# Optimization experiments

Hardware: AMD Instinct MI355X
Metric: run time of the kernel (lower is better)

The kernel has to match this reference:

```python
import jax, jax.numpy as jnp
import numpy as np

B, S, D, H, DH, DM = 2, 2048, 1024, 16, 64, 4096
EPS = 1e-5
IGNORE = -100000.0
INIT_RANGE = 0.02


def setup_inputs() -> dict:
    key = jax.random.key(0)
    ks = jax.random.split(key, 8)
    inp = {
        "resid_pre": jax.random.normal(ks[0], (B, S, D), jnp.float32),
        "ln1_w": jnp.ones((D,), jnp.float32),
        "ln1_b": jnp.zeros((D,), jnp.float32),
        "W_Q": jax.random.normal(ks[1], (H, D, DH), jnp.float32) * 0.05,
        "b_Q": jnp.zeros((H, DH), jnp.float32),
        "W_K": jax.random.normal(ks[2], (H, D, DH), jnp.float32) * 0.05,
        "b_K": jnp.zeros((H, DH), jnp.float32),
        "W_V": jax.random.normal(ks[3], (H, D, DH), jnp.float32) * 0.05,
        "b_V": jnp.zeros((H, DH), jnp.float32),
        "W_O": jax.random.normal(ks[4], (H, DH, D), jnp.float32) * 0.05,
        "b_O": jnp.zeros((D,), jnp.float32),
        "ln2_w": jnp.ones((D,), jnp.float32),
        "ln2_b": jnp.zeros((D,), jnp.float32),
        "W_in": jax.random.normal(ks[5], (D, DM), jnp.float32) * INIT_RANGE,
        "b_in": jnp.zeros((DM,), jnp.float32),
        "W_out": jax.random.normal(ks[6], (DM, D), jnp.float32) * INIT_RANGE,
        "b_out": jnp.zeros((D,), jnp.float32),
    }
    return inp


def _layernorm(x, w, b):
    mean = jnp.mean(x, axis=-1, keepdims=True)
    xc = x - mean
    var = jnp.mean(jnp.square(xc), axis=-1, keepdims=True)
    return xc / jnp.sqrt(var + EPS) * w + b


def _attention(x, W_Q, b_Q, W_K, b_K, W_V, b_V, W_O, b_O):
    q = jnp.einsum('bqd,hdm->bqhm', x, W_Q) + b_Q
    k = jnp.einsum('bkd,hdm->bkhm', x, W_K) + b_K
    scores = jnp.einsum('bqhd,bkhd->bhqk', q, k) / jnp.sqrt(jnp.float32(DH))
    s = x.shape[1]
    causal = jnp.tril(jnp.ones((s, s), bool))  # True = keep
    scores = jnp.where(causal, scores, IGNORE)
    pattern = jax.nn.softmax(scores, axis=-1)
    v = jnp.einsum('bkd,hdm->bkhm', x, W_V) + b_V
    z = jnp.einsum('bhqk,bkhd->bqhd', pattern, v)
    return jnp.einsum('bqhd,hdm->bqm', z, W_O) + b_O


def reference(resid_pre, ln1_w, ln1_b, W_Q, b_Q, W_K, b_K, W_V, b_V, W_O, b_O,
              ln2_w, ln2_b, W_in, b_in, W_out, b_out):
    # Pre-LN attention + residual (dropout disabled: inference mode)
    attn_out = _attention(_layernorm(resid_pre, ln1_w, ln1_b),
                          W_Q, b_Q, W_K, b_K, W_V, b_V, W_O, b_O)
    resid_mid = resid_pre + attn_out
    # Pre-LN MLP + residual; keras gelu default is exact (erf-based)
    h = _layernorm(resid_mid, ln2_w, ln2_b)
    pre = jnp.einsum('bpd,dm->bpm', h, W_in) + b_in
    post = jax.nn.gelu(pre, approximate=False)
    mlp_out = jnp.einsum('bpm,md->bpd', post, W_out) + b_out
    return resid_mid + mlp_out
```

## Files before the change

### kernel.cpp

```cpp
#include <hip/hip_runtime.h>
#include <math.h>

#define S_LEN   2048
#define D_MODEL 1024
#define N_HEADS 16
#define D_HEAD  64
#define D_MLP   4096
#define T_TOKENS 4096
#define QSCALE_F 0.18033688011112042f

typedef __attribute__((ext_vector_type(8))) short short8;
typedef __attribute__((ext_vector_type(4))) float f32x4;
typedef unsigned short ushort_t;
typedef unsigned long long u64;

__device__ __forceinline__ ushort_t f2bf(float x) {
    unsigned int u = __float_as_uint(x);
    return (ushort_t)((u + 0x7FFFu + ((u >> 16) & 1u)) >> 16);
}

__device__ __forceinline__ float gelu_exact(float x) {
    return 0.5f * x * (1.0f + erff(x * 0.7071067811865476f));
}

__device__ __forceinline__ void gld_lds16(const void* g, void* l) {
    __builtin_amdgcn_global_load_lds(
        (const __attribute__((address_space(1))) unsigned int*)g,
        (__attribute__((address_space(3))) unsigned int*)l, 16, 0, 0);
}

__device__ __forceinline__ void swizzle_mn(int& m0, int& n0) {
    int gx = gridDim.x;
    int b = blockIdx.y * gx + blockIdx.x;
    int band = b & 7, t = b >> 3;
    n0 = (t % gx) * 128;
    m0 = (band * 4 + t / gx) * 128;
}


__global__ __launch_bounds__(256) void ln_kernel(const float* __restrict__ x,
                                                 const float* __restrict__ w,
                                                 const float* __restrict__ b,
                                                 ushort_t* __restrict__ out) {
    int t = blockIdx.x;
    int tid = threadIdx.x;
    const float* xp = x + (size_t)t * D_MODEL;
    float4 v = *(const float4*)(xp + tid * 4);
    float s  = v.x + v.y + v.z + v.w;
    float sq = v.x*v.x + v.y*v.y + v.z*v.z + v.w*v.w;
    for (int o = 32; o; o >>= 1) {
        s  += __shfl_down(s, o, 64);
        sq += __shfl_down(sq, o, 64);
    }
    __shared__ float ss[4], ssq[4];
    if ((tid & 63) == 0) { ss[tid >> 6] = s; ssq[tid >> 6] = sq; }
    __syncthreads();
    float S  = ss[0] + ss[1] + ss[2] + ss[3];
    float SQ = ssq[0] + ssq[1] + ssq[2] + ssq[3];
    float mean = S * (1.0f / D_MODEL);
    float var  = SQ * (1.0f / D_MODEL) - mean * mean;
    float rstd = rsqrtf(var + 1e-5f);
    float4 wv = *(const float4*)(w + tid * 4);
    float4 bv = *(const float4*)(b + tid * 4);
    float ox = (v.x - mean) * rstd * wv.x + bv.x;
    float oy = (v.y - mean) * rstd * wv.y + bv.y;
    float oz = (v.z - mean) * rstd * wv.z + bv.z;
    float ow = (v.w - mean) * rstd * wv.w + bv.w;
    u64 pack = (u64)f2bf(ox) | ((u64)f2bf(oy) << 16) | ((u64)f2bf(oz) << 32) | ((u64)f2bf(ow) << 48);
    *(u64*)(out + (size_t)t * D_MODEL + tid * 4) = pack;
}

__global__ __launch_bounds__(256) void transpose_f2b(const float* __restrict__ in,
                                                     long long inStride, int ldin,
                                                     ushort_t* __restrict__ out,
                                                     long long outStride, int ldout) {
    in  += (size_t)blockIdx.z * inStride;
    out += (size_t)blockIdx.z * outStride;
    __shared__ float t[32][33];
    int c0 = blockIdx.x * 32, r0 = blockIdx.y * 32;
    int tx = threadIdx.x, ty = threadIdx.y;
    #pragma unroll
    for (int i = 0; i < 32; i += 8)
        t[ty + i][tx] = in[(size_t)(r0 + ty + i) * ldin + c0 + tx];
    __syncthreads();
    #pragma unroll
    for (int i = 0; i < 32; i += 8)
        out[(size_t)(c0 + ty + i) * ldout + r0 + tx] = f2bf(t[tx][ty + i]);
}

__global__ __launch_bounds__(256) void tpose_b2b(const ushort_t* __restrict__ in,
                                                 ushort_t* __restrict__ out) {
    int pair = blockIdx.z;
    in  += (size_t)pair * (S_LEN * 64);
    out += (size_t)pair * (S_LEN * 64);
    __shared__ ushort_t t[32][33];
    int s0 = blockIdx.x * 32, d0 = blockIdx.y * 32;
    int tx = threadIdx.x, ty = threadIdx.y;
    #pragma unroll
    for (int i = 0; i < 32; i += 8)
        t[ty + i][tx] = in[(size_t)(s0 + ty + i) * 64 + d0 + tx];
    __syncthreads();
    #pragma unroll
    for (int i = 0; i < 32; i += 8)
        out[(size_t)(d0 + ty + i) * S_LEN + s0 + tx] = t[tx][ty + i];
}

__global__ __launch_bounds__(256) void qkv_bias_cat(const float* __restrict__ bq,
                                                    const float* __restrict__ bk,
                                                    const float* __restrict__ bv,
                                                    float* __restrict__ out) {
    int i = blockIdx.x * 256 + threadIdx.x;
    float v = (i < 1024) ? bq[i] : (i < 2048 ? bk[i - 1024] : bv[i - 2048]);
    out[i] = v;
}

template<int OUT_MODE, bool DO_GELU, bool HAS_RES>
__global__ __launch_bounds__(256, 4) void mfma_gemm(
    const ushort_t* __restrict__ A, int lda,
    const ushort_t* __restrict__ Bt, int ldb,
    void* __restrict__ Cv, int ldc, int K,
    const float* __restrict__ bias,
    const float* __restrict__ res, int ldres) {

    __shared__ ushort_t As[2][128 * 32];
    __shared__ ushort_t Bs[2][128 * 32];

    int tid  = threadIdx.x;
    int lane = tid & 63;
    int m0, n0;
    swizzle_mn(m0, n0);
    int wave = tid >> 6;
    int wm = (wave & 1) * 64, wn = (wave >> 1) * 64;
    int quad = lane >> 4, l15 = lane & 15;

    int srow = tid >> 2;
    int skc  = (((tid & 3) ^ ((tid >> 3) & 3))) * 8;
    const ushort_t* Ap  = A  + (size_t)(m0 + srow)      * lda + skc;
    const ushort_t* Ap2 = A  + (size_t)(m0 + srow + 64) * lda + skc;
    const ushort_t* Bp  = Bt + (size_t)(n0 + srow)      * ldb + skc;
    const ushort_t* Bp2 = Bt + (size_t)(n0 + srow + 64) * ldb + skc;

    int fsw = (l15 >> 1) & 3;

    f32x4 acc[4][4];
    #pragma unroll
    for (int i = 0; i < 4; ++i)
        #pragma unroll
        for (int j = 0; j < 4; ++j)
            acc[i][j] = (f32x4){0.f, 0.f, 0.f, 0.f};

    gld_lds16(Ap,  &As[0][tid * 8]);
    gld_lds16(Ap2, &As[0][(tid + 256) * 8]);
    gld_lds16(Bp,  &Bs[0][tid * 8]);
    gld_lds16(Bp2, &Bs[0][(tid + 256) * 8]);

    int niter = K >> 5;
    for (int j = 0; j < niter; ++j) {
        __syncthreads();
        int p = j & 1;
        if (j + 1 < niter) {
            int k1 = (j + 1) << 5;
            gld_lds16(Ap  + k1, &As[p ^ 1][tid * 8]);
            gld_lds16(Ap2 + k1, &As[p ^ 1][(tid + 256) * 8]);
            gld_lds16(Bp  + k1, &Bs[p ^ 1][tid * 8]);
            gld_lds16(Bp2 + k1, &Bs[p ^ 1][(tid + 256) * 8]);
        }
        short8 a[4], b[4];
        #pragma unroll
        for (int i = 0; i < 4; ++i) {
            a[i] = *(const short8*)&As[p][(wm + i * 16 + l15) * 32 + (quad ^ fsw) * 8];
            b[i] = *(const short8*)&Bs[p][(wn + i * 16 + l15) * 32 + (quad ^ fsw) * 8];
        }
        #pragma unroll
        for (int i = 0; i < 4; ++i)
            #pragma unroll
            for (int jj = 0; jj < 4; ++jj)
                acc[i][jj] = __builtin_amdgcn_mfma_f32_16x16x32_bf16(a[i], b[jj], acc[i][jj], 0, 0, 0);
    }

    #pragma unroll
    for (int i = 0; i < 4; ++i) {
        int rBase = m0 + wm + i * 16 + quad * 4;
        #pragma unroll
        for (int j = 0; j < 4; ++j) {
            int col = n0 + wn + j * 16 + l15;
            float bv = bias ? bias[col] : 0.f;
            #pragma unroll
            for (int r = 0; r < 4; ++r) {
                int rowg = rBase + r;
                float v = acc[i][j][r] + bv;
                if (DO_GELU) v = gelu_exact(v);
                if (HAS_RES) v += res[(size_t)rowg * ldres + col];
                if (OUT_MODE == 0)
                    ((float*)Cv)[(size_t)rowg * ldc + col] = v;
                else
                    ((ushort_t*)Cv)[(size_t)rowg * ldc + col] = f2bf(v);
            }
        }
    }
}

template<int OUT_MODE, bool DO_GELU, bool HAS_RES>
__global__ __launch_bounds__(512, 2) void mfma_gemm_sk(
    const ushort_t* __restrict__ A, int lda,
    const ushort_t* __restrict__ Bt, int ldb,
    void* __restrict__ Cv, int ldc, int K,
    const float* __restrict__ bias,
    const float* __restrict__ res, int ldres) {

    __shared__ ushort_t Smem[32768];
    #define SA_(g, p) (Smem + ((g) * 2 + (p)) * 4096)
    #define SB_(g, p) (Smem + 16384 + ((g) * 2 + (p)) * 4096)

    int tid  = threadIdx.x;
    int lane = tid & 63;
    int wave = tid >> 6;
    int g = wave >> 2, w = wave & 3;
    int m0, n0;
    swizzle_mn(m0, n0);
    int wm = (w & 1) * 64, wn = (w >> 1) * 64;
    int quad = lane >> 4, l15 = lane & 15;

    int lt = tid & 255;
    int srow = lt >> 2;
    int skc  = (((lt & 3) ^ ((lt >> 3) & 3))) * 8;
    int kbase = g * (K >> 1);
    const ushort_t* Ap  = A  + (size_t)(m0 + srow)      * lda + kbase + skc;
    const ushort_t* Ap2 = A  + (size_t)(m0 + srow + 64) * lda + kbase + skc;
    const ushort_t* Bp  = Bt + (size_t)(n0 + srow)      * ldb + kbase + skc;
    const ushort_t* Bp2 = Bt + (size_t)(n0 + srow + 64) * ldb + kbase + skc;

    int fsw = (l15 >> 1) & 3;

    f32x4 acc[4][4];
    #pragma unroll
    for (int i = 0; i < 4; ++i)
        #pragma unroll
        for (int j = 0; j < 4; ++j)
            acc[i][j] = (f32x4){0.f, 0.f, 0.f, 0.f};

    gld_lds16(Ap,  SA_(g, 0) + lt * 8);
    gld_lds16(Ap2, SA_(g, 0) + (lt + 256) * 8);
    gld_lds16(Bp,  SB_(g, 0) + lt * 8);
    gld_lds16(Bp2, SB_(g, 0) + (lt + 256) * 8);

    int niter = K >> 6;
    for (int j = 0; j < niter; ++j) {
        __syncthreads();
        int p = j & 1;
        if (j + 1 < niter) {
            int k1 = (j + 1) << 5;
            gld_lds16(Ap  + k1, SA_(g, p ^ 1) + lt * 8);
            gld_lds16(Ap2 + k1, SA_(g, p ^ 1) + (lt + 256) * 8);
            gld_lds16(Bp  + k1, SB_(g, p ^ 1) + lt * 8);
            gld_lds16(Bp2 + k1, SB_(g, p ^ 1) + (lt + 256) * 8);
        }
        const ushort_t* Ac = SA_(g, p);
        const ushort_t* Bc = SB_(g, p);
        short8 a[4], b[4];
        #pragma unroll
        for (int i = 0; i < 4; ++i) {
            a[i] = *(const short8*)(Ac + (wm + i * 16 + l15) * 32 + (quad ^ fsw) * 8);
            b[i] = *(const short8*)(Bc + (wn + i * 16 + l15) * 32 + (quad ^ fsw) * 8);
        }
        #pragma unroll
        for (int i = 0; i < 4; ++i)
            #pragma unroll
            for (int jj = 0; jj < 4; ++jj)
                acc[i][jj] = __builtin_amdgcn_mfma_f32_16x16x32_bf16(a[i], b[jj], acc[i][jj], 0, 0, 0);
    }

    __syncthreads();
    float* R = (float*)Smem;
    if (g == 1) {
        #pragma unroll
        for (int i = 0; i < 4; ++i)
            #pragma unroll
            for (int j = 0; j < 4; ++j)
                *(f32x4*)&R[(((w * 16 + i * 4 + j) * 64) + lane) * 4] = acc[i][j];
    }
    __syncthreads();
    if (g == 0) {
        #pragma unroll
        for (int i = 0; i < 4; ++i) {
            int rBase = m0 + wm + i * 16 + quad * 4;
            #pragma unroll
            for (int j = 0; j < 4; ++j) {
                f32x4 other = *(const f32x4*)&R[(((w * 16 + i * 4 + j) * 64) + lane) * 4];
                int col = n0 + wn + j * 16 + l15;
                float bv = bias ? bias[col] : 0.f;
                #pragma unroll
                for (int r = 0; r < 4; ++r) {
                    int rowg = rBase + r;
                    float v = acc[i][j][r] + other[r] + bv;
                    if (DO_GELU) v = gelu_exact(v);
                    if (HAS_RES) v += res[(size_t)rowg * ldres + col];
                    if (OUT_MODE == 0)
                        ((float*)Cv)[(size_t)rowg * ldc + col] = v;
                    else
                        ((ushort_t*)Cv)[(size_t)rowg * ldc + col] = f2bf(v);
                }
            }
        }
    }
    #undef SA_
    #undef SB_
}

__global__ __launch_bounds__(256, 4) void mfma_gemm_qkv(
    const ushort_t* __restrict__ A, const ushort_t* __restrict__ Bt,
    ushort_t* __restrict__ Qh, ushort_t* __restrict__ Kh, ushort_t* __restrict__ Vh,
    const float* __restrict__ bias) {

    const int lda = 1024, ldb = 1024, K = 1024;
    __shared__ ushort_t As[2][128 * 32];
    __shared__ ushort_t Bs[2][128 * 32];

    int tid  = threadIdx.x;
    int lane = tid & 63;
    int m0, n0;
    swizzle_mn(m0, n0);
    int wave = tid >> 6;
    int wm = (wave & 1) * 64, wn = (wave >> 1) * 64;
    int quad = lane >> 4, l15 = lane & 15;

    int srow = tid >> 2;
    int skc  = (((tid & 3) ^ ((tid >> 3) & 3))) * 8;
    const ushort_t* Ap  = A  + (size_t)(m0 + srow)      * lda + skc;
    const ushort_t* Ap2 = A  + (size_t)(m0 + srow + 64) * lda + skc;
    const ushort_t* Bp  = Bt + (size_t)(n0 + srow)      * ldb + skc;
    const ushort_t* Bp2 = Bt + (size_t)(n0 + srow + 64) * ldb + skc;

    int fsw = (l15 >> 1) & 3;

    f32x4 acc[4][4];
    #pragma unroll
    for (int i = 0; i < 4; ++i)
        #pragma unroll
        for (int j = 0; j < 4; ++j)
            acc[i][j] = (f32x4){0.f, 0.f, 0.f, 0.f};

    gld_lds16(Ap,  &As[0][tid * 8]);
    gld_lds16(Ap2, &As[0][(tid + 256) * 8]);
    gld_lds16(Bp,  &Bs[0][tid * 8]);
    gld_lds16(Bp2, &Bs[0][(tid + 256) * 8]);

    const int niter = K >> 5;
    for (int j = 0; j < niter; ++j) {
        __syncthreads();
        int p = j & 1;
        if (j + 1 < niter) {
            int k1 = (j + 1) << 5;
            gld_lds16(Ap  + k1, &As[p ^ 1][tid * 8]);
            gld_lds16(Ap2 + k1, &As[p ^ 1][(tid + 256) * 8]);
            gld_lds16(Bp  + k1, &Bs[p ^ 1][tid * 8]);
            gld_lds16(Bp2 + k1, &Bs[p ^ 1][(tid + 256) * 8]);
        }
        short8 a[4], b[4];
        #pragma unroll
        for (int i = 0; i < 4; ++i) {
            a[i] = *(const short8*)&As[p][(wm + i * 16 + l15) * 32 + (quad ^ fsw) * 8];
            b[i] = *(const short8*)&Bs[p][(wn + i * 16 + l15) * 32 + (quad ^ fsw) * 8];
        }
        #pragma unroll
        for (int i = 0; i < 4; ++i)
            #pragma unroll
            for (int jj = 0; jj < 4; ++jj)
                acc[i][jj] = __builtin_amdgcn_mfma_f32_16x16x32_bf16(a[i], b[jj], acc[i][jj], 0, 0, 0);
    }

    #pragma unroll
    for (int i = 0; i < 4; ++i) {
        int rBase = m0 + wm + i * 16 + quad * 4;
        #pragma unroll
        for (int j = 0; j < 4; ++j) {
            int col = n0 + wn + j * 16 + l15;
            int sel = col >> 10;
            int h   = (col >> 6) & 15;
            int dh  = col & 63;
            ushort_t* dst = (sel == 0) ? Qh : (sel == 1 ? Kh : Vh);
            float sc = (sel == 0) ? QSCALE_F : 1.0f;
            float bv = bias[col];
            #pragma unroll
            for (int r = 0; r < 4; ++r) {
                int rowg = rBase + r;
                int bb = rowg >> 11, s = rowg & 2047;
                float v = (acc[i][j][r] + bv) * sc;
                dst[((size_t)(bb * 16 + h) * S_LEN + s) * 64 + dh] = f2bf(v);
            }
        }
    }
}

__global__ __launch_bounds__(256, 4) void flash_kernel(
    const ushort_t* __restrict__ Qh, const ushort_t* __restrict__ Kh,
    const ushort_t* __restrict__ Vt, ushort_t* __restrict__ Z) {

    __shared__ ushort_t Klds[2][64 * 64];
    __shared__ ushort_t Vlds[2][64 * 64];
    __shared__ ushort_t Plds[4][16 * 64];

    int pair = blockIdx.x;
    int qt   = blockIdx.y;
    int q0   = qt * 64;
    int tid = threadIdx.x, lane = tid & 63, wave = tid >> 6;
    int quad = lane >> 4, l15 = lane & 15;

    const ushort_t* Qbase = Qh + (size_t)pair * (S_LEN * 64);
    const ushort_t* Kbase = Kh + (size_t)pair * (S_LEN * 64);
    const ushort_t* Vbase = Vt + (size_t)pair * (S_LEN * 64);
    ushort_t* Qstage = &Plds[0][0];

    #pragma unroll
    for (int n = 0; n < 2; ++n) {
        int c = tid + n * 256;
        int row = c >> 3, part = c & 7;
        gld_lds16(Qbase + (size_t)(q0 + row) * 64 + ((part ^ (row & 7)) * 8), Qstage + c * 8);
    }
    __syncthreads();
    short8 qa[2];
    #pragma unroll
    for (int h = 0; h < 2; ++h) {
        int row = wave * 16 + l15;
        int part = (h * 4 + quad) ^ (row & 7);
        qa[h] = *(const short8*)(Qstage + row * 64 + part * 8);
    }

    f32x4 ls = (f32x4){0.f, 0.f, 0.f, 0.f};
    f32x4 zacc[4];
    #pragma unroll
    for (int dht = 0; dht < 4; ++dht) zacc[dht] = (f32x4){0.f, 0.f, 0.f, 0.f};

    #pragma unroll
    for (int n = 0; n < 2; ++n) {
        int c = tid + n * 256;
        int row = c >> 3, part = c & 7;
        int gp = (part ^ (row & 7)) * 8;
        gld_lds16(Kbase + (size_t)row * 64 + gp, &Klds[0][0] + c * 8);
        gld_lds16(Vbase + (size_t)row * S_LEN + gp, &Vlds[0][0] + c * 8);
    }

    for (int j = 0; j <= qt; ++j) {
        __syncthreads();
        int p = j & 1;
        if (j < qt) {
            int k1 = (j + 1) * 64;
            #pragma unroll
            for (int n = 0; n < 2; ++n) {
                int c = tid + n * 256;
                int row = c >> 3, part = c & 7;
                int gp = (part ^ (row & 7)) * 8;
                gld_lds16(Kbase + (size_t)(k1 + row) * 64 + gp, &Klds[p ^ 1][0] + c * 8);
                gld_lds16(Vbase + (size_t)row * S_LEN + k1 + gp, &Vlds[p ^ 1][0] + c * 8);
            }
        }
        const ushort_t* Kc = &Klds[p][0];
        const ushort_t* Vc = &Vlds[p][0];

        f32x4 s[4];
        #pragma unroll
        for (int jt = 0; jt < 4; ++jt) {
            int krow = jt * 16 + l15;
            int sw = krow & 7;
            short8 kb0 = *(const short8*)(Kc + krow * 64 + ((quad ^ sw) * 8));
            short8 kb1 = *(const short8*)(Kc + krow * 64 + (((quad + 4) ^ sw) * 8));
            f32x4 t = __builtin_amdgcn_mfma_f32_16x16x32_bf16(qa[0], kb0,
                        (f32x4){0.f, 0.f, 0.f, 0.f}, 0, 0, 0);
            s[jt] = __builtin_amdgcn_mfma_f32_16x16x32_bf16(qa[1], kb1, t, 0, 0, 0);
        }

        if (j == qt) {
            #pragma unroll
            for (int jt = 0; jt < 4; ++jt) {
                int kc = jt * 16 + l15;
                int qr = wave * 16 + quad * 4;
                #pragma unroll
                for (int r = 0; r < 4; ++r)
                    if (kc > qr + r) s[jt][r] = -1e30f;
            }
        }

        #pragma unroll
        for (int jt = 0; jt < 4; ++jt) {
            #pragma unroll
            for (int r = 0; r < 4; ++r) {
                float pv = exp2f(s[jt][r]);
                s[jt][r] = pv;
                ls[r] += pv;
            }
        }

        ushort_t* Pw = &Plds[wave][0];
        #pragma unroll
        for (int jt = 0; jt < 4; ++jt) {
            int col = jt * 16 + l15;
            int cp = col >> 3, ci = col & 7;
            #pragma unroll
            for (int r = 0; r < 4; ++r) {
                int prow = quad * 4 + r;
                Pw[prow * 64 + ((cp ^ (prow & 7)) * 8) + ci] = f2bf(s[jt][r]);
            }
        }

        #pragma unroll
        for (int kc = 0; kc < 2; ++kc) {
            int prow = l15;
            short8 pa = *(const short8*)(Pw + prow * 64 + ((((kc * 4 + quad) ^ (prow & 7))) * 8));
            #pragma unroll
            for (int dht = 0; dht < 4; ++dht) {
                int vrow = dht * 16 + l15;
                short8 vb = *(const short8*)(Vc + vrow * 64 + ((((kc * 4 + quad) ^ (vrow & 7))) * 8));
                zacc[dht] = __builtin_amdgcn_mfma_f32_16x16x32_bf16(pa, vb, zacc[dht], 0, 0, 0);
            }
        }
    }

    #pragma unroll
    for (int d = 1; d < 16; d <<= 1) {
        ls[0] += __shfl_xor(ls[0], d, 64);
        ls[1] += __shfl_xor(ls[1], d, 64);
        ls[2] += __shfl_xor(ls[2], d, 64);
        ls[3] += __shfl_xor(ls[3], d, 64);
    }
    int bb = pair >> 4, h = pair & 15;
    #pragma unroll
    for (int r = 0; r < 4; ++r) {
        int qrow = q0 + wave * 16 + quad * 4 + r;
        size_t tok = (size_t)bb * S_LEN + qrow;
        float inv = 1.0f / ls[r];
        #pragma unroll
        for (int dht = 0; dht < 4; ++dht)
            Z[tok * D_MODEL + h * 64 + dht * 16 + l15] = f2bf(zacc[dht][r] * inv);
    }
}

extern "C" void kernel_launch(void* const* d_in, const int* in_sizes, int n_in,
                              void* d_out, int out_size, void* d_ws, size_t ws_size,
                              hipStream_t stream) {
    const float* resid_pre = (const float*)d_in[0];
    const float* ln1_w = (const float*)d_in[1];
    const float* ln1_b = (const float*)d_in[2];
    const float* W_Q   = (const float*)d_in[3];
    const float* b_Q   = (const float*)d_in[4];
    const float* W_K   = (const float*)d_in[5];
    const float* b_K   = (const float*)d_in[6];
    const float* W_V   = (const float*)d_in[7];
    const float* b_V   = (const float*)d_in[8];
    const float* W_O   = (const float*)d_in[9];
    const float* b_O   = (const float*)d_in[10];
    const float* ln2_w = (const float*)d_in[11];
    const float* ln2_b = (const float*)d_in[12];
    const float* W_in  = (const float*)d_in[13];
    const float* b_in  = (const float*)d_in[14];
    const float* W_out = (const float*)d_in[15];
    const float* b_out = (const float*)d_in[16];
    float* out = (float*)d_out;
    char* W = (char*)d_ws;

    const size_t MB = 1u << 20;
    ushort_t* Qh     = (ushort_t*)(W + 0 * MB);
    ushort_t* Kh     = (ushort_t*)(W + 8 * MB);
    ushort_t* Vh     = (ushort_t*)(W + 16 * MB);
    ushort_t* Vt     = (ushort_t*)(W + 24 * MB);
    ushort_t* Zbf    = (ushort_t*)(W + 32 * MB);
    ushort_t* LN1a   = (ushort_t*)(W + 40 * MB);
    ushort_t* Wqkv   = (ushort_t*)(W + 48 * MB);
    ushort_t* Wo_t   = (ushort_t*)(W + 54 * MB);
    ushort_t* Win_t  = (ushort_t*)(W + 56 * MB);
    ushort_t* Wout_t = (ushort_t*)(W + 64 * MB);
    ushort_t* LN2a   = (ushort_t*)(W + 72 * MB);
    ushort_t* MLPh   = (ushort_t*)(W + 80 * MB);
    float*    MID    = (float*)  (W + 112 * MB);
    float*    qbias  = (float*)  (W + 128 * MB);

    const size_t M1 = 1u << 20;
    dim3 tb(32, 8);

    transpose_f2b<<<dim3(2, 32, 16), tb, 0, stream>>>(W_Q, 65536, 64, Wqkv,          65536, 1024);
    transpose_f2b<<<dim3(2, 32, 16), tb, 0, stream>>>(W_K, 65536, 64, Wqkv + 1 * M1, 65536, 1024);
    transpose_f2b<<<dim3(2, 32, 16), tb, 0, stream>>>(W_V, 65536, 64, Wqkv + 2 * M1, 65536, 1024);
    qkv_bias_cat<<<12, 256, 0, stream>>>(b_Q, b_K, b_V, qbias);
    ln_kernel<<<T_TOKENS, 256, 0, stream>>>(resid_pre, ln1_w, ln1_b, LN1a);

    mfma_gemm_qkv<<<dim3(24, 32), 256, 0, stream>>>(LN1a, Wqkv, Qh, Kh, Vh, qbias);
    tpose_b2b<<<dim3(64, 2, 32), tb, 0, stream>>>(Vh, Vt);

    flash_kernel<<<dim3(32, 32), 256, 0, stream>>>(Qh, Kh, Vt, Zbf);

    transpose_f2b<<<dim3(32, 32, 1), tb, 0, stream>>>(W_O, 0, 1024, Wo_t, 0, 1024);
    mfma_gemm_sk<0, false, true><<<dim3(8, 32), 512, 0, stream>>>(
        Zbf, 1024, Wo_t, 1024, MID, 1024, 1024, b_O, resid_pre, 1024);

    ln_kernel<<<T_TOKENS, 256, 0, stream>>>(MID, ln2_w, ln2_b, LN2a);
    transpose_f2b<<<dim3(128, 32, 1), tb, 0, stream>>>(W_in,  0, 4096, Win_t,  0, 1024);
    transpose_f2b<<<dim3(32, 128, 1), tb, 0, stream>>>(W_out, 0, 1024, Wout_t, 0, 4096);
    mfma_gemm<1, true, false><<<dim3(32, 32), 256, 0, stream>>>(
        LN2a, 1024, Win_t, 1024, MLPh, 4096, 1024, b_in, nullptr, 0);
    mfma_gemm_sk<0, false, true><<<dim3(8, 32), 512, 0, stream>>>(
        MLPh, 4096, Wout_t, 4096, out, 1024, 4096, b_out, MID, 1024);
}
```

Measured before the change: 377.5 us.

## Merge weight prep kernels, store residual mid in bf16, widen split-K GEMM k-tile

Folds all weight transposes and the bias concat into a single prep_weights launch, cutting several small launches. The intermediate residual stream is now stored as bf16 instead of fp32, with a new bf16 layernorm and a bf16 residual add in the final GEMM, which halves that traffic but rounds the residual to bf16. The split-K GEMM now uses a 64-wide k tile with a new XOR swizzle and 128KB of shared memory at occupancy 1, so it needs fewer loop iterations and barriers but keeps fewer blocks resident per CU.

```diff
diff --git a/kernel.cpp b/kernel.cpp
--- a/kernel.cpp
+++ b/kernel.cpp
@@ -18,6 +18,10 @@
     unsigned int u = __float_as_uint(x);
     return (ushort_t)((u + 0x7FFFu + ((u >> 16) & 1u)) >> 16);
 }
+__device__ __forceinline__ float bf2f(ushort_t x) {
+    unsigned int u = ((unsigned int)x) << 16;
+    return __uint_as_float(u);
+}
 
 __device__ __forceinline__ float gelu_exact(float x) {
     return 0.5f * x * (1.0f + erff(x * 0.7071067811865476f));
@@ -36,7 +40,6 @@
     n0 = (t % gx) * 128;
     m0 = (band * 4 + t / gx) * 128;
 }
-
 
 __global__ __launch_bounds__(256) void ln_kernel(const float* __restrict__ x,
                                                  const float* __restrict__ w,
@@ -70,15 +73,77 @@
     *(u64*)(out + (size_t)t * D_MODEL + tid * 4) = pack;
 }
 
-__global__ __launch_bounds__(256) void transpose_f2b(const float* __restrict__ in,
-                                                     long long inStride, int ldin,
-                                                     ushort_t* __restrict__ out,
-                                                     long long outStride, int ldout) {
-    in  += (size_t)blockIdx.z * inStride;
-    out += (size_t)blockIdx.z * outStride;
+__global__ __launch_bounds__(256) void ln_kernel_b(const ushort_t* __restrict__ x,
+                                                   const float* __restrict__ w,
+                                                   const float* __restrict__ b,
+                                                   ushort_t* __restrict__ out) {
+    int t = blockIdx.x;
+    int tid = threadIdx.x;
+    const ushort_t* xp = x + (size_t)t * D_MODEL;
+    u64 pk = *(const u64*)(xp + tid * 4);
+    float vx = bf2f((ushort_t)(pk & 0xffff));
+    float vy = bf2f((ushort_t)((pk >> 16) & 0xffff));
+    float vz = bf2f((ushort_t)((pk >> 32) & 0xffff));
+    float vw = bf2f((ushort_t)(pk >> 48));
+    float s  = vx + vy + vz + vw;
+    float sq = vx*vx + vy*vy + vz*vz + vw*vw;
+    for (int o = 32; o; o >>= 1) {
+        s  += __shfl_down(s, o, 64);
+        sq += __shfl_down(sq, o, 64);
+    }
+    __shared__ float ss[4], ssq[4];
+    if ((tid & 63) == 0) { ss[tid >> 6] = s; ssq[tid >> 6] = sq; }
+    __syncthreads();
+    float S  = ss[0] + ss[1] + ss[2] + ss[3];
+    float SQ = ssq[0] + ssq[1] + ssq[2] + ssq[3];
+    float mean = S * (1.0f / D_MODEL);
+    float var  = SQ * (1.0f / D_MODEL) - mean * mean;
+    float rstd = rsqrtf(var + 1e-5f);
+    float4 wv = *(const float4*)(w + tid * 4);
+    float4 bv = *(const float4*)(b + tid * 4);
+    float ox = (vx - mean) * rstd * wv.x + bv.x;
+    float oy = (vy - mean) * rstd * wv.y + bv.y;
+    float oz = (vz - mean) * rstd * wv.z + bv.z;
+    float ow = (vw - mean) * rstd * wv.w + bv.w;
+    u64 pack = (u64)f2bf(ox) | ((u64)f2bf(oy) << 16) | ((u64)f2bf(oz) << 32) | ((u64)f2bf(ow) << 48);
+    *(u64*)(out + (size_t)t * D_MODEL + tid * 4) = pack;
+}
+
+__global__ __launch_bounds__(256) void prep_weights(
+    const float* __restrict__ Wq, const float* __restrict__ Wk, const float* __restrict__ Wv,
+    const float* __restrict__ Wo, const float* __restrict__ Wi, const float* __restrict__ Wu,
+    const float* __restrict__ bq, const float* __restrict__ bk, const float* __restrict__ bv,
+    ushort_t* __restrict__ wqkv, ushort_t* __restrict__ wo_t,
+    ushort_t* __restrict__ win_t, ushort_t* __restrict__ wout_t,
+    float* __restrict__ qbias) {
+    int blk = blockIdx.x;
+    if (blk >= 12288) {
+        int i = (blk - 12288) * 256 + threadIdx.x;
+        float v = (i < 1024) ? bq[i] : (i < 2048 ? bk[i - 1024] : bv[i - 2048]);
+        qbias[i] = v;
+        return;
+    }
+    int tx = threadIdx.x & 31, ty = threadIdx.x >> 5;
+    const float* in; ushort_t* out; int ldin, ldout, bx, by;
+    if (blk < 3072) {
+        int w = blk >> 10, r = blk & 1023;
+        int z = r >> 6; r &= 63;
+        bx = r & 1; by = r >> 1;
+        in  = (w == 0 ? Wq : (w == 1 ? Wk : Wv)) + (size_t)z * 65536;
+        out = wqkv + (size_t)w * (1u << 20) + (size_t)z * 65536;
+        ldin = 64; ldout = 1024;
+    } else if (blk < 4096) {
+        int r = blk - 3072; bx = r & 31; by = r >> 5;
+        in = Wo; out = wo_t; ldin = 1024; ldout = 1024;
+    } else if (blk < 8192) {
+        int r = blk - 4096; bx = r & 127; by = r >> 7;
+        in = Wi; out = win_t; ldin = 4096; ldout = 1024;
+    } else {
+        int r = blk - 8192; bx = r & 31; by = r >> 5;
+        in = Wu; out = wout_t; ldin = 1024; ldout = 4096;
+    }
     __shared__ float t[32][33];
-    int c0 = blockIdx.x * 32, r0 = blockIdx.y * 32;
-    int tx = threadIdx.x, ty = threadIdx.y;
+    int c0 = bx * 32, r0 = by * 32;
     #pragma unroll
     for (int i = 0; i < 32; i += 8)
         t[ty + i][tx] = in[(size_t)(r0 + ty + i) * ldin + c0 + tx];
@@ -105,22 +170,13 @@
         out[(size_t)(d0 + ty + i) * S_LEN + s0 + tx] = t[tx][ty + i];
 }
 
-__global__ __launch_bounds__(256) void qkv_bias_cat(const float* __restrict__ bq,
-                                                    const float* __restrict__ bk,
-                                                    const float* __restrict__ bv,
-                                                    float* __restrict__ out) {
-    int i = blockIdx.x * 256 + threadIdx.x;
-    float v = (i < 1024) ? bq[i] : (i < 2048 ? bk[i - 1024] : bv[i - 2048]);
-    out[i] = v;
-}
-
-template<int OUT_MODE, bool DO_GELU, bool HAS_RES>
+template<int OUT_MODE, bool DO_GELU, int RES_MODE>
 __global__ __launch_bounds__(256, 4) void mfma_gemm(
     const ushort_t* __restrict__ A, int lda,
     const ushort_t* __restrict__ Bt, int ldb,
     void* __restrict__ Cv, int ldc, int K,
     const float* __restrict__ bias,
-    const float* __restrict__ res, int ldres) {
+    const void* __restrict__ res, int ldres) {
 
     __shared__ ushort_t As[2][128 * 32];
     __shared__ ushort_t Bs[2][128 * 32];
@@ -190,7 +246,8 @@
                 int rowg = rBase + r;
                 float v = acc[i][j][r] + bv;
                 if (DO_GELU) v = gelu_exact(v);
-                if (HAS_RES) v += res[(size_t)rowg * ldres + col];
+                if (RES_MODE == 1) v += ((const float*)res)[(size_t)rowg * ldres + col];
+                if (RES_MODE == 2) v += bf2f(((const ushort_t*)res)[(size_t)rowg * ldres + col]);
                 if (OUT_MODE == 0)
                     ((float*)Cv)[(size_t)rowg * ldc + col] = v;
                 else
@@ -200,17 +257,17 @@
     }
 }
 
-template<int OUT_MODE, bool DO_GELU, bool HAS_RES>
-__global__ __launch_bounds__(512, 2) void mfma_gemm_sk(
+template<int OUT_MODE, bool DO_GELU, int RES_MODE>
+__global__ __launch_bounds__(512, 1) void mfma_gemm_sk(
     const ushort_t* __restrict__ A, int lda,
     const ushort_t* __restrict__ Bt, int ldb,
     void* __restrict__ Cv, int ldc, int K,
     const float* __restrict__ bias,
-    const float* __restrict__ res, int ldres) {
-
-    __shared__ ushort_t Smem[32768];
-    #define SA_(g, p) (Smem + ((g) * 2 + (p)) * 4096)
-    #define SB_(g, p) (Smem + 16384 + ((g) * 2 + (p)) * 4096)
+    const void* __restrict__ res, int ldres) {
+
+    __shared__ ushort_t Smem[65536];
+    #define SA_(g, p) (Smem + ((g) * 2 + (p)) * 8192)
+    #define SB_(g, p) (Smem + 32768 + ((g) * 2 + (p)) * 8192)
 
     int tid  = threadIdx.x;
     int lane = tid & 63;
@@ -222,15 +279,11 @@
     int quad = lane >> 4, l15 = lane & 15;
 
     int lt = tid & 255;
-    int srow = lt >> 2;
-    int skc  = (((lt & 3) ^ ((lt >> 3) & 3))) * 8;
+    int srow = lt >> 3;
+    int gp8  = ((lt & 7) ^ (srow & 7)) * 8;
     int kbase = g * (K >> 1);
-    const ushort_t* Ap  = A  + (size_t)(m0 + srow)      * lda + kbase + skc;
-    const ushort_t* Ap2 = A  + (size_t)(m0 + srow + 64) * lda + kbase + skc;
-    const ushort_t* Bp  = Bt + (size_t)(n0 + srow)      * ldb + kbase + skc;
-    const ushort_t* Bp2 = Bt + (size_t)(n0 + srow + 64) * ldb + kbase + skc;
-
-    int fsw = (l15 >> 1) & 3;
+    const ushort_t* ApB = A  + (size_t)m0 * lda + kbase + gp8;
+    const ushort_t* BpB = Bt + (size_t)n0 * ldb + kbase + gp8;
 
     f32x4 acc[4][4];
     #pragma unroll
@@ -239,35 +292,44 @@
         for (int j = 0; j < 4; ++j)
             acc[i][j] = (f32x4){0.f, 0.f, 0.f, 0.f};
 
-    gld_lds16(Ap,  SA_(g, 0) + lt * 8);
-    gld_lds16(Ap2, SA_(g, 0) + (lt + 256) * 8);
-    gld_lds16(Bp,  SB_(g, 0) + lt * 8);
-    gld_lds16(Bp2, SB_(g, 0) + (lt + 256) * 8);
-
-    int niter = K >> 6;
+    #pragma unroll
+    for (int n = 0; n < 4; ++n) {
+        int row = n * 32 + srow;
+        gld_lds16(ApB + (size_t)row * lda, SA_(g, 0) + (n * 256 + lt) * 8);
+        gld_lds16(BpB + (size_t)row * ldb, SB_(g, 0) + (n * 256 + lt) * 8);
+    }
+
+    int niter = K >> 7;
     for (int j = 0; j < niter; ++j) {
         __syncthreads();
         int p = j & 1;
         if (j + 1 < niter) {
-            int k1 = (j + 1) << 5;
-            gld_lds16(Ap  + k1, SA_(g, p ^ 1) + lt * 8);
-            gld_lds16(Ap2 + k1, SA_(g, p ^ 1) + (lt + 256) * 8);
-            gld_lds16(Bp  + k1, SB_(g, p ^ 1) + lt * 8);
-            gld_lds16(Bp2 + k1, SB_(g, p ^ 1) + (lt + 256) * 8);
+            int k1 = (j + 1) << 6;
+            #pragma unroll
+            for (int n = 0; n < 4; ++n) {
+                int row = n * 32 + srow;
+                gld_lds16(ApB + (size_t)row * lda + k1, SA_(g, p ^ 1) + (n * 256 + lt) * 8);
+                gld_lds16(BpB + (size_t)row * ldb + k1, SB_(g, p ^ 1) + (n * 256 + lt) * 8);
+            }
         }
         const ushort_t* Ac = SA_(g, p);
         const ushort_t* Bc = SB_(g, p);
-        short8 a[4], b[4];
-        #pragma unroll
-        for (int i = 0; i < 4; ++i) {
-            a[i] = *(const short8*)(Ac + (wm + i * 16 + l15) * 32 + (quad ^ fsw) * 8);
-            b[i] = *(const short8*)(Bc + (wn + i * 16 + l15) * 32 + (quad ^ fsw) * 8);
-        }
-        #pragma unroll
-        for (int i = 0; i < 4; ++i)
-            #pragma unroll
-            for (int jj = 0; jj < 4; ++jj)
-                acc[i][jj] = __builtin_amdgcn_mfma_f32_16x16x32_bf16(a[i], b[jj], acc[i][jj], 0, 0, 0);
+        #pragma unroll
+        for (int kk = 0; kk < 2; ++kk) {
+            short8 a[4], b[4];
+            #pragma unroll
+            for (int i = 0; i < 4; ++i) {
+                int ra = wm + i * 16 + l15;
+                int rb = wn + i * 16 + l15;
+                a[i] = *(const short8*)(Ac + ra * 64 + (((kk * 4 + quad) ^ (ra & 7))) * 8);
+                b[i] = *(const short8*)(Bc + rb * 64 + (((kk * 4 + quad) ^ (rb & 7))) * 8);
+            }
+            #pragma unroll
+            for (int i = 0; i < 4; ++i)
+                #pragma unroll
+                for (int jj = 0; jj < 4; ++jj)
+                    acc[i][jj] = __builtin_amdgcn_mfma_f32_16x16x32_bf16(a[i], b[jj], acc[i][jj], 0, 0, 0);
+        }
     }
 
     __syncthreads();
@@ -294,7 +356,8 @@
                     int rowg = rBase + r;
                     float v = acc[i][j][r] + other[r] + bv;
                     if (DO_GELU) v = gelu_exact(v);
-                    if (HAS_RES) v += res[(size_t)rowg * ldres + col];
+                    if (RES_MODE == 1) v += ((const float*)res)[(size_t)rowg * ldres + col];
+                    if (RES_MODE == 2) v += bf2f(((const ushort_t*)res)[(size_t)rowg * ldres + col]);
                     if (OUT_MODE == 0)
                         ((float*)Cv)[(size_t)rowg * ldc + col] = v;
                     else
@@ -570,16 +633,14 @@
     ushort_t* Wout_t = (ushort_t*)(W + 64 * MB);
     ushort_t* LN2a   = (ushort_t*)(W + 72 * MB);
     ushort_t* MLPh   = (ushort_t*)(W + 80 * MB);
-    float*    MID    = (float*)  (W + 112 * MB);
+    ushort_t* MIDb   = (ushort_t*)(W + 112 * MB);
     float*    qbias  = (float*)  (W + 128 * MB);
 
-    const size_t M1 = 1u << 20;
     dim3 tb(32, 8);
 
-    transpose_f2b<<<dim3(2, 32, 16), tb, 0, stream>>>(W_Q, 65536, 64, Wqkv,          65536, 1024);
-    transpose_f2b<<<dim3(2, 32, 16), tb, 0, stream>>>(W_K, 65536, 64, Wqkv + 1 * M1, 65536, 1024);
-    transpose_f2b<<<dim3(2, 32, 16), tb, 0, stream>>>(W_V, 65536, 64, Wqkv + 2 * M1, 65536, 1024);
-    qkv_bias_cat<<<12, 256, 0, stream>>>(b_Q, b_K, b_V, qbias);
+    prep_weights<<<12300, 256, 0, stream>>>(W_Q, W_K, W_V, W_O, W_in, W_out,
+                                            b_Q, b_K, b_V,
+                                            Wqkv, Wo_t, Win_t, Wout_t, qbias);
     ln_kernel<<<T_TOKENS, 256, 0, stream>>>(resid_pre, ln1_w, ln1_b, LN1a);
 
     mfma_gemm_qkv<<<dim3(24, 32), 256, 0, stream>>>(LN1a, Wqkv, Qh, Kh, Vh, qbias);
@@ -587,15 +648,12 @@
 
     flash_kernel<<<dim3(32, 32), 256, 0, stream>>>(Qh, Kh, Vt, Zbf);
 
-    transpose_f2b<<<dim3(32, 32, 1), tb, 0, stream>>>(W_O, 0, 1024, Wo_t, 0, 1024);
-    mfma_gemm_sk<0, false, true><<<dim3(8, 32), 512, 0, stream>>>(
-        Zbf, 1024, Wo_t, 1024, MID, 1024, 1024, b_O, resid_pre, 1024);
-
-    ln_kernel<<<T_TOKENS, 256, 0, stream>>>(MID, ln2_w, ln2_b, LN2a);
-    transpose_f2b<<<dim3(128, 32, 1), tb, 0, stream>>>(W_in,  0, 4096, Win_t,  0, 1024);
-    transpose_f2b<<<dim3(32, 128, 1), tb, 0, stream>>>(W_out, 0, 1024, Wout_t, 0, 4096);
-    mfma_gemm<1, true, false><<<dim3(32, 32), 256, 0, stream>>>(
+    mfma_gemm_sk<1, false, 1><<<dim3(8, 32), 512, 0, stream>>>(
+        Zbf, 1024, Wo_t, 1024, MIDb, 1024, 1024, b_O, resid_pre, 1024);
+
+    ln_kernel_b<<<T_TOKENS, 256, 0, stream>>>(MIDb, ln2_w, ln2_b, LN2a);
+    mfma_gemm<1, true, 0><<<dim3(32, 32), 256, 0, stream>>>(
         LN2a, 1024, Win_t, 1024, MLPh, 4096, 1024, b_in, nullptr, 0);
-    mfma_gemm_sk<0, false, true><<<dim3(8, 32), 512, 0, stream>>>(
-        MLPh, 4096, Wout_t, 4096, out, 1024, 4096, b_out, MID, 1024);
-}
+    mfma_gemm_sk<0, false, 2><<<dim3(8, 32), 512, 0, stream>>>(
+        MLPh, 4096, Wout_t, 4096, out, 1024, 4096, b_out, MIDb, 1024);
+}
```

Result: faster. 343.5 us (-9.0%).
